# Performance work log

Measured on AMD Instinct MI355X. Metric: run time of the kernel, lower is better.

## Reference

```python
import jax, jax.numpy as jnp
import numpy as np

B, DIN, NS, NF = 2048, 512, 256, 64

def setup_inputs() -> dict:
    key = jax.random.key(0)
    ks = jax.random.split(key, 16)
    s = 0.05
    return {
        'x_i': jax.random.normal(ks[0], (B, DIN), jnp.float32),
        'h_i': jax.random.normal(ks[1], (B, NS), jnp.float32),
        'S_i': jax.random.normal(ks[2], (B, 2, NS, NF), jnp.float32),
        'W_fste': jax.random.normal(ks[3], (DIN + NS, NS), jnp.float32) * s,
        'b_fste': jnp.zeros((NS,), jnp.float32),
        'W_ffreq': jax.random.normal(ks[4], (DIN + NS, NF), jnp.float32) * s,
        'b_ffreq': jnp.zeros((NF,), jnp.float32),
        'W_i': jax.random.normal(ks[5], (DIN + NS, NS), jnp.float32) * s,
        'b_i': jnp.zeros((NS,), jnp.float32),
        'W_c': jax.random.normal(ks[6], (DIN + NS, NS), jnp.float32) * s,
        'b_c': jnp.zeros((NS,), jnp.float32),
        'u_a': jax.random.normal(ks[7], (NF,), jnp.float32) * s,
        'b_a': jnp.zeros((NS,), jnp.float32),
        'W_o': jax.random.normal(ks[8], (DIN + NS + NS, NS), jnp.float32) * s,
        'b_o': jnp.zeros((NS,), jnp.float32),
        't': 3,
    }

def reference(x_i, h_i, S_i, W_fste, b_fste, W_ffreq, b_ffreq, W_i, b_i, W_c, b_c, u_a, b_a, W_o, b_o, t):
    nf = u_a.shape[0]
    # angle = ((arange(nf)*t) % nf) / (nf / (2*pi))  -- matches np precedence in source
    ang = ((jnp.arange(nf, dtype=jnp.float32) * t) % nf) * (2.0 * jnp.pi / nf)
    omega = jnp.stack([jnp.sin(ang), jnp.cos(ang)])[:, None]        # [2,1,nf]
    x_h = jnp.concatenate([x_i, h_i], axis=-1)                      # [B, DIN+NS]
    f_ste = jax.nn.sigmoid(x_h @ W_fste + b_fste)                   # [B,NS]
    f_freq = jax.nn.sigmoid(x_h @ W_ffreq + b_ffreq)                # [B,NF]
    F_t = jnp.einsum('bi,bj->bij', f_ste, f_freq)                   # [B,NS,NF]
    i_dot = jax.nn.sigmoid(x_h @ W_i + b_i)                         # [B,NS]
    c_wave = jnp.tanh(x_h @ W_c + b_c)                              # [B,NS]
    i_c_omega = (i_dot * c_wave)[:, None, :, None] * omega          # [B,2,NS,NF]
    S_next = S_i * F_t[:, None] + i_c_omega                         # [B,2,NS,NF]
    A_i = jnp.sqrt(jnp.sum(S_next ** 2, axis=1))                    # [B,NS,NF]
    c_t = jax.nn.sigmoid(jnp.einsum('bij,j->bi', A_i, u_a) + b_a)   # [B,NS]
    o_i = jax.nn.sigmoid(jnp.concatenate([x_h, c_t], -1) @ W_o + b_o)
    h_next = o_i * c_t
    return h_next, S_next
```

## Files before the change

kernel.cpp:

```cpp
#include <hip/hip_runtime.h>
#include <math.h>

#define BATCH 2048
#define DIN   512
#define NS    256
#define NF    64
#define KG    768
#define NG    832
#define KO    1024

__device__ __forceinline__ float sigmoidf_(float x) { return 1.0f / (1.0f + expf(-x)); }

__global__ __launch_bounds__(256) void gates_gemm(
    const float* __restrict__ x, const float* __restrict__ h,
    const float* __restrict__ Wf, const float* __restrict__ bf,
    const float* __restrict__ Wq, const float* __restrict__ bq,
    const float* __restrict__ Wi, const float* __restrict__ bi,
    const float* __restrict__ Wc, const float* __restrict__ bc,
    float* __restrict__ gates)
{
    __shared__ float As[64][33];
    __shared__ float Bs[32][65];

    const int nt = blockIdx.x;
    const int mt = blockIdx.y;
    const int t  = threadIdx.x;

    const int n0 = nt * 64;
    const float* Wp; const float* bp; int ld, noff, act;
    if (n0 < 256)      { Wp = Wf; bp = bf; ld = 256; noff = 0;   act = 0; }
    else if (n0 < 320) { Wp = Wq; bp = bq; ld = 64;  noff = 256; act = 0; }
    else if (n0 < 576) { Wp = Wi; bp = bi; ld = 256; noff = 320; act = 0; }
    else               { Wp = Wc; bp = bc; ld = 256; noff = 576; act = 1; }
    const int nloc0 = n0 - noff;

    const int tx = t & 15, ty = t >> 4;
    const int m0 = mt * 64;
    float acc[4][4] = {};

    for (int kt = 0; kt < KG; kt += 32) {
        #pragma unroll
        for (int it = 0; it < 8; ++it) {
            int lin = t + 256 * it;
            int row = lin >> 5, kk = lin & 31;
            int m = m0 + row, k = kt + kk;
            As[row][kk] = (k < DIN) ? x[m * DIN + k] : h[m * NS + (k - DIN)];
        }
        #pragma unroll
        for (int it = 0; it < 8; ++it) {
            int lin = t + 256 * it;
            int kk = lin >> 6, ni = lin & 63;
            Bs[kk][ni] = Wp[(kt + kk) * ld + nloc0 + ni];
        }
        __syncthreads();
        #pragma unroll
        for (int kk = 0; kk < 32; ++kk) {
            float a[4], bv[4];
            #pragma unroll
            for (int r = 0; r < 4; ++r) a[r] = As[ty * 4 + r][kk];
            #pragma unroll
            for (int c = 0; c < 4; ++c) bv[c] = Bs[kk][tx * 4 + c];
            #pragma unroll
            for (int r = 0; r < 4; ++r)
                #pragma unroll
                for (int c = 0; c < 4; ++c)
                    acc[r][c] = fmaf(a[r], bv[c], acc[r][c]);
        }
        __syncthreads();
    }

    #pragma unroll
    for (int r = 0; r < 4; ++r) {
        int m = m0 + ty * 4 + r;
        #pragma unroll
        for (int c = 0; c < 4; ++c) {
            int nl = nloc0 + tx * 4 + c;
            float v = acc[r][c] + bp[nl];
            v = act ? tanhf(v) : sigmoidf_(v);
            gates[m * NG + n0 + tx * 4 + c] = v;
        }
    }
}

__global__ __launch_bounds__(256) void supdate(
    const float* __restrict__ S, const float* __restrict__ gates,
    const float* __restrict__ ua, const float* __restrict__ ba,
    const int* __restrict__ tptr,
    float* __restrict__ Sout, float* __restrict__ ct)
{
    const int tid = blockIdx.x * 256 + threadIdx.x;
    const int q    = tid & 15;
    const int pair = tid >> 4;
    const int b = pair >> 8, s = pair & 255;
    const int f0 = q * 4;
    const int tv = *tptr;

    const float* grow = gates + b * NG;
    const float fste = grow[s];
    const float ic   = grow[320 + s] * grow[576 + s];

    const float4 ff  = *(const float4*)(grow + 256 + f0);
    const float4 ua4 = *(const float4*)(ua + f0);

    const size_t base0 = (((size_t)b * 2 + 0) * NS + s) * NF + f0;
    const size_t base1 = (((size_t)b * 2 + 1) * NS + s) * NF + f0;
    const float4 si0 = *(const float4*)(S + base0);
    const float4 si1 = *(const float4*)(S + base1);

    float fv[4] = { ff.x, ff.y, ff.z, ff.w };
    float uv[4] = { ua4.x, ua4.y, ua4.z, ua4.w };
    float a0[4] = { si0.x, si0.y, si0.z, si0.w };
    float a1[4] = { si1.x, si1.y, si1.z, si1.w };

    float part = 0.0f;
    float o0[4], o1[4];
    #pragma unroll
    for (int j = 0; j < 4; ++j) {
        int f = f0 + j;
        float ang = (float)((f * tv) & (NF - 1)) * (float)(M_PI / 32.0);
        float sn, cs;
        sincosf(ang, &sn, &cs);
        float F = fste * fv[j];
        float u = a0[j] * F + ic * sn;
        float v = a1[j] * F + ic * cs;
        o0[j] = u; o1[j] = v;
        part += sqrtf(u * u + v * v) * uv[j];
    }
    *(float4*)(Sout + base0) = make_float4(o0[0], o0[1], o0[2], o0[3]);
    *(float4*)(Sout + base1) = make_float4(o1[0], o1[1], o1[2], o1[3]);

    part += __shfl_xor(part, 1);
    part += __shfl_xor(part, 2);
    part += __shfl_xor(part, 4);
    part += __shfl_xor(part, 8);
    if (q == 0) ct[pair] = sigmoidf_(part + ba[s]);
}

__global__ __launch_bounds__(256) void out_gemm(
    const float* __restrict__ x, const float* __restrict__ h,
    const float* __restrict__ ct,
    const float* __restrict__ Wo, const float* __restrict__ bo,
    float* __restrict__ hout)
{
    __shared__ float As[64][33];
    __shared__ float Bs[32][65];

    const int nt = blockIdx.x;
    const int mt = blockIdx.y;
    const int t  = threadIdx.x;
    const int n0 = nt * 64;
    const int tx = t & 15, ty = t >> 4;
    const int m0 = mt * 64;
    float acc[4][4] = {};

    for (int kt = 0; kt < KO; kt += 32) {
        #pragma unroll
        for (int it = 0; it < 8; ++it) {
            int lin = t + 256 * it;
            int row = lin >> 5, kk = lin & 31;
            int m = m0 + row, k = kt + kk;
            float v;
            if (k < DIN)           v = x[m * DIN + k];
            else if (k < DIN + NS) v = h[m * NS + (k - DIN)];
            else                   v = ct[m * NS + (k - DIN - NS)];
            As[row][kk] = v;
        }
        #pragma unroll
        for (int it = 0; it < 8; ++it) {
            int lin = t + 256 * it;
            int kk = lin >> 6, ni = lin & 63;
            Bs[kk][ni] = Wo[(kt + kk) * NS + n0 + ni];
        }
        __syncthreads();
        #pragma unroll
        for (int kk = 0; kk < 32; ++kk) {
            float a[4], bv[4];
            #pragma unroll
            for (int r = 0; r < 4; ++r) a[r] = As[ty * 4 + r][kk];
            #pragma unroll
            for (int c = 0; c < 4; ++c) bv[c] = Bs[kk][tx * 4 + c];
            #pragma unroll
            for (int r = 0; r < 4; ++r)
                #pragma unroll
                for (int c = 0; c < 4; ++c)
                    acc[r][c] = fmaf(a[r], bv[c], acc[r][c]);
        }
        __syncthreads();
    }

    #pragma unroll
    for (int r = 0; r < 4; ++r) {
        int m = m0 + ty * 4 + r;
        #pragma unroll
        for (int c = 0; c < 4; ++c) {
            int n = n0 + tx * 4 + c;
            float o = sigmoidf_(acc[r][c] + bo[n]);
            hout[m * NS + n] = o * ct[m * NS + n];
        }
    }
}

extern "C" void kernel_launch(void* const* d_in, const int* in_sizes, int n_in,
                              void* d_out, int out_size, void* d_ws, size_t ws_size,
                              hipStream_t stream)
{
    const float* x  = (const float*)d_in[0];
    const float* h  = (const float*)d_in[1];
    const float* S  = (const float*)d_in[2];
    const float* Wf = (const float*)d_in[3];
    const float* bf = (const float*)d_in[4];
    const float* Wq = (const float*)d_in[5];
    const float* bq = (const float*)d_in[6];
    const float* Wi = (const float*)d_in[7];
    const float* bi = (const float*)d_in[8];
    const float* Wc = (const float*)d_in[9];
    const float* bc = (const float*)d_in[10];
    const float* ua = (const float*)d_in[11];
    const float* ba = (const float*)d_in[12];
    const float* Wo = (const float*)d_in[13];
    const float* bo = (const float*)d_in[14];
    const int*   tp = (const int*)d_in[15];

    float* gates = (float*)d_ws;
    float* ct    = gates + (size_t)BATCH * NG;
    float* hout  = (float*)d_out;
    float* Sout  = hout + (size_t)BATCH * NS;

    gates_gemm<<<dim3(13, 32), 256, 0, stream>>>(x, h, Wf, bf, Wq, bq, Wi, bi, Wc, bc, gates);
    supdate<<<dim3((BATCH * NS * 16) / 256), 256, 0, stream>>>(S, gates, ua, ba, tp, Sout, ct);
    out_gemm<<<dim3(4, 32), 256, 0, stream>>>(x, h, ct, Wo, bo, hout);
}
```

Baseline: 696.5 us.

## Vectorize GEMM tile loads with transposed A in LDS and use fast intrinsics

Both GEMM kernels now stage 16-wide K tiles with float4 global loads. A is stored transposed in shared memory so the inner loop reads A and B fragments as float4 LDS loads instead of scalar strided reads. The sigmoid switches to __expf and the S-update uses __sinf/__cosf, trading a little accuracy for cheaper transcendentals. The halved K tile doubles the number of barrier pairs per GEMM, and the transposed A stores into LDS may cause bank conflicts.

```diff
diff --git a/kernel.cpp b/kernel.cpp
--- a/kernel.cpp
+++ b/kernel.cpp
@@ -9,18 +9,18 @@
 #define NG    832
 #define KO    1024
 
-__device__ __forceinline__ float sigmoidf_(float x) { return 1.0f / (1.0f + expf(-x)); }
+__device__ __forceinline__ float sigmoidf_(float x) { return 1.0f / (1.0f + __expf(-x)); }
 
 __global__ __launch_bounds__(256) void gates_gemm(
     const float* __restrict__ x, const float* __restrict__ h,
     const float* __restrict__ Wf, const float* __restrict__ bf,
     const float* __restrict__ Wq, const float* __restrict__ bq,
     const float* __restrict__ Wi, const float* __restrict__ bi,
-    const float* __restrict__ Wc, const float* __restrict__ bc,
+    const float* __restrict__ Wc, const float* __restrict__ bcg,
     float* __restrict__ gates)
 {
-    __shared__ float As[64][33];
-    __shared__ float Bs[32][65];
+    __shared__ float As[16][68];
+    __shared__ float Bs[16][68];
 
     const int nt = blockIdx.x;
     const int mt = blockIdx.y;
@@ -28,56 +28,59 @@
 
     const int n0 = nt * 64;
     const float* Wp; const float* bp; int ld, noff, act;
-    if (n0 < 256)      { Wp = Wf; bp = bf; ld = 256; noff = 0;   act = 0; }
-    else if (n0 < 320) { Wp = Wq; bp = bq; ld = 64;  noff = 256; act = 0; }
-    else if (n0 < 576) { Wp = Wi; bp = bi; ld = 256; noff = 320; act = 0; }
-    else               { Wp = Wc; bp = bc; ld = 256; noff = 576; act = 1; }
+    if (n0 < 256)      { Wp = Wf; bp = bf;  ld = 256; noff = 0;   act = 0; }
+    else if (n0 < 320) { Wp = Wq; bp = bq;  ld = 64;  noff = 256; act = 0; }
+    else if (n0 < 576) { Wp = Wi; bp = bi;  ld = 256; noff = 320; act = 0; }
+    else               { Wp = Wc; bp = bcg; ld = 256; noff = 576; act = 1; }
     const int nloc0 = n0 - noff;
 
     const int tx = t & 15, ty = t >> 4;
     const int m0 = mt * 64;
+
+    const int ar = t >> 2;
+    const int ak = (t & 3) * 4;
+    const int bk   = t >> 4;
+    const int bcol = (t & 15) * 4;
+
     float acc[4][4] = {};
 
-    for (int kt = 0; kt < KG; kt += 32) {
-        #pragma unroll
-        for (int it = 0; it < 8; ++it) {
-            int lin = t + 256 * it;
-            int row = lin >> 5, kk = lin & 31;
-            int m = m0 + row, k = kt + kk;
-            As[row][kk] = (k < DIN) ? x[m * DIN + k] : h[m * NS + (k - DIN)];
-        }
-        #pragma unroll
-        for (int it = 0; it < 8; ++it) {
-            int lin = t + 256 * it;
-            int kk = lin >> 6, ni = lin & 63;
-            Bs[kk][ni] = Wp[(kt + kk) * ld + nloc0 + ni];
-        }
-        __syncthreads();
-        #pragma unroll
-        for (int kk = 0; kk < 32; ++kk) {
-            float a[4], bv[4];
-            #pragma unroll
-            for (int r = 0; r < 4; ++r) a[r] = As[ty * 4 + r][kk];
-            #pragma unroll
-            for (int c = 0; c < 4; ++c) bv[c] = Bs[kk][tx * 4 + c];
+    for (int kt = 0; kt < KG; kt += 16) {
+        {
+            const int k = kt + ak;
+            const int m = m0 + ar;
+            float4 a4 = (k < DIN) ? *(const float4*)(x + (size_t)m * DIN + k)
+                                  : *(const float4*)(h + (size_t)m * NS + (k - DIN));
+            As[ak + 0][ar] = a4.x; As[ak + 1][ar] = a4.y;
+            As[ak + 2][ar] = a4.z; As[ak + 3][ar] = a4.w;
+        }
+        *(float4*)&Bs[bk][bcol] = *(const float4*)(Wp + (size_t)(kt + bk) * ld + nloc0 + bcol);
+        __syncthreads();
+
+        #pragma unroll
+        for (int kk = 0; kk < 16; ++kk) {
+            float4 a = *(const float4*)&As[kk][ty * 4];
+            float4 b = *(const float4*)&Bs[kk][tx * 4];
+            float av[4] = { a.x, a.y, a.z, a.w };
+            float bv[4] = { b.x, b.y, b.z, b.w };
             #pragma unroll
             for (int r = 0; r < 4; ++r)
                 #pragma unroll
                 for (int c = 0; c < 4; ++c)
-                    acc[r][c] = fmaf(a[r], bv[c], acc[r][c]);
-        }
-        __syncthreads();
-    }
-
+                    acc[r][c] = fmaf(av[r], bv[c], acc[r][c]);
+        }
+        __syncthreads();
+    }
+
+    const float4 bb = *(const float4*)(bp + nloc0 + tx * 4);
+    const float bvv[4] = { bb.x, bb.y, bb.z, bb.w };
     #pragma unroll
     for (int r = 0; r < 4; ++r) {
-        int m = m0 + ty * 4 + r;
+        const int m = m0 + ty * 4 + r;
         #pragma unroll
         for (int c = 0; c < 4; ++c) {
-            int nl = nloc0 + tx * 4 + c;
-            float v = acc[r][c] + bp[nl];
+            float v = acc[r][c] + bvv[c];
             v = act ? tanhf(v) : sigmoidf_(v);
-            gates[m * NG + n0 + tx * 4 + c] = v;
+            gates[(size_t)m * NG + n0 + tx * 4 + c] = v;
         }
     }
 }
@@ -95,7 +98,7 @@
     const int f0 = q * 4;
     const int tv = *tptr;
 
-    const float* grow = gates + b * NG;
+    const float* grow = gates + (size_t)b * NG;
     const float fste = grow[s];
     const float ic   = grow[320 + s] * grow[576 + s];
 
@@ -118,8 +121,7 @@
     for (int j = 0; j < 4; ++j) {
         int f = f0 + j;
         float ang = (float)((f * tv) & (NF - 1)) * (float)(M_PI / 32.0);
-        float sn, cs;
-        sincosf(ang, &sn, &cs);
+        float sn = __sinf(ang), cs = __cosf(ang);
         float F = fste * fv[j];
         float u = a0[j] * F + ic * sn;
         float v = a1[j] * F + ic * cs;
@@ -142,8 +144,8 @@
     const float* __restrict__ Wo, const float* __restrict__ bo,
     float* __restrict__ hout)
 {
-    __shared__ float As[64][33];
-    __shared__ float Bs[32][65];
+    __shared__ float As[16][68];
+    __shared__ float Bs[16][68];
 
     const int nt = blockIdx.x;
     const int mt = blockIdx.y;
@@ -151,51 +153,51 @@
     const int n0 = nt * 64;
     const int tx = t & 15, ty = t >> 4;
     const int m0 = mt * 64;
+
+    const int ar = t >> 2;
+    const int ak = (t & 3) * 4;
+    const int bk   = t >> 4;
+    const int bcol = (t & 15) * 4;
+
     float acc[4][4] = {};
 
-    for (int kt = 0; kt < KO; kt += 32) {
-        #pragma unroll
-        for (int it = 0; it < 8; ++it) {
-            int lin = t + 256 * it;
-            int row = lin >> 5, kk = lin & 31;
-            int m = m0 + row, k = kt + kk;
-            float v;
-            if (k < DIN)           v = x[m * DIN + k];
-            else if (k < DIN + NS) v = h[m * NS + (k - DIN)];
-            else                   v = ct[m * NS + (k - DIN - NS)];
-            As[row][kk] = v;
-        }
-        #pragma unroll
-        for (int it = 0; it < 8; ++it) {
-            int lin = t + 256 * it;
-            int kk = lin >> 6, ni = lin & 63;
-            Bs[kk][ni] = Wo[(kt + kk) * NS + n0 + ni];
-        }
-        __syncthreads();
-        #pragma unroll
-        for (int kk = 0; kk < 32; ++kk) {
-            float a[4], bv[4];
-            #pragma unroll
-            for (int r = 0; r < 4; ++r) a[r] = As[ty * 4 + r][kk];
-            #pragma unroll
-            for (int c = 0; c < 4; ++c) bv[c] = Bs[kk][tx * 4 + c];
+    for (int kt = 0; kt < KO; kt += 16) {
+        {
+            const int k = kt + ak;
+            const int m = m0 + ar;
+            float4 a4;
+            if (k < DIN)           a4 = *(const float4*)(x  + (size_t)m * DIN + k);
+            else if (k < DIN + NS) a4 = *(const float4*)(h  + (size_t)m * NS + (k - DIN));
+            else                   a4 = *(const float4*)(ct + (size_t)m * NS + (k - DIN - NS));
+            As[ak + 0][ar] = a4.x; As[ak + 1][ar] = a4.y;
+            As[ak + 2][ar] = a4.z; As[ak + 3][ar] = a4.w;
+        }
+        *(float4*)&Bs[bk][bcol] = *(const float4*)(Wo + (size_t)(kt + bk) * NS + n0 + bcol);
+        __syncthreads();
+
+        #pragma unroll
+        for (int kk = 0; kk < 16; ++kk) {
+            float4 a = *(const float4*)&As[kk][ty * 4];
+            float4 b = *(const float4*)&Bs[kk][tx * 4];
+            float av[4] = { a.x, a.y, a.z, a.w };
+            float bv[4] = { b.x, b.y, b.z, b.w };
             #pragma unroll
             for (int r = 0; r < 4; ++r)
                 #pragma unroll
                 for (int c = 0; c < 4; ++c)
-                    acc[r][c] = fmaf(a[r], bv[c], acc[r][c]);
+                    acc[r][c] = fmaf(av[r], bv[c], acc[r][c]);
         }
         __syncthreads();
     }
 
     #pragma unroll
     for (int r = 0; r < 4; ++r) {
-        int m = m0 + ty * 4 + r;
+        const int m = m0 + ty * 4 + r;
         #pragma unroll
         for (int c = 0; c < 4; ++c) {
-            int n = n0 + tx * 4 + c;
+            const int n = n0 + tx * 4 + c;
             float o = sigmoidf_(acc[r][c] + bo[n]);
-            hout[m * NS + n] = o * ct[m * NS + n];
+            hout[(size_t)m * NS + n] = o * ct[(size_t)m * NS + n];
         }
     }
 }
```

Result: faster. 603.1 us (-13.4%).
